# Kernel optimization log

Hardware: AMD Instinct MI355X
Metric: run time of the kernel (lower is better)

Reference implementation:

```python
import jax, jax.numpy as jnp
import numpy as np
from jax import lax

B, N, T, H = 128, 2, 256, 128  # batch, inc_nodes, seq_len, lstm hidden


def setup_inputs() -> dict:
    key = jax.random.key(0)
    ks = jax.random.split(key, 20)
    r = lambda i, shape, s: (jax.random.normal(ks[i], shape) * s).astype(jnp.float32)
    return {
        "x": r(0, (B, N, T), 1.0),
        "h0": r(1, (N, 4, B, H), 1.0),   # (node, layer*D+dir, B, H), torch.randn init states
        "c0": r(2, (N, 4, B, H), 1.0),
        "w_ih0": r(3, (N, 2, 4 * H, 1), 0.05),
        "w_hh0": r(4, (N, 2, 4 * H, H), 0.05),
        "b0": r(5, (N, 2, 4 * H), 0.05),
        "w_ih1": r(6, (N, 2, 4 * H, 2 * H), 0.05),
        "w_hh1": r(7, (N, 2, 4 * H, H), 0.05),
        "b1": r(8, (N, 2, 4 * H), 0.05),
        "w_fc0": r(9, (N * 2 * H, 256), 0.05), "b_fc0": r(10, (256,), 0.05),
        "ln0_a": r(11, (256,), 1.0), "ln0_b": r(12, (256,), 1.0),
        "w_fc1": r(13, (256, 256), 0.05), "b_fc1": r(14, (256,), 0.05),
        "ln1_a": r(15, (256,), 1.0), "ln1_b": r(16, (256,), 1.0),
        "w_fc2": r(17, (256, 64), 0.05), "b_fc2": r(18, (64,), 0.05),
    }


def _lstm_dir(xp, h0, c0, w_hh):
    # xp: [T, B, 4H] precomputed input projections + bias; returns [T, B, H]
    def step(hc, xt):
        h, c = hc
        g = xt + h @ w_hh.T
        i, f, gg, o = jnp.split(g, 4, axis=-1)  # torch gate order i,f,g,o
        c = jax.nn.sigmoid(f) * c + jax.nn.sigmoid(i) * jnp.tanh(gg)
        h = jax.nn.sigmoid(o) * jnp.tanh(c)
        return (h, c), h
    _, hs = lax.scan(step, (h0, c0), xp)
    return hs


def _bidir(x, h0, c0, w_ih, w_hh, b):
    # x: [B,T,Din]; h0,c0: [2,B,H]; w_ih: [2,4H,Din]; w_hh: [2,4H,H]; b: [2,4H]
    xp_f = jnp.moveaxis(x @ w_ih[0].T + b[0], 1, 0)            # [T,B,4H]
    hf = _lstm_dir(xp_f, h0[0], c0[0], w_hh[0])
    xp_b = jnp.moveaxis(x[:, ::-1] @ w_ih[1].T + b[1], 1, 0)
    hb = _lstm_dir(xp_b, h0[1], c0[1], w_hh[1])[::-1]
    return jnp.moveaxis(jnp.concatenate([hf, hb], axis=-1), 0, 1)  # [B,T,2H]


def _node(xn, h0n, c0n, wi0, wh0, bb0, wi1, wh1, bb1):
    # xn: [B,T,1]; h0n/c0n: [4,B,H] laid out (l0f, l0b, l1f, l1b)
    y = _bidir(xn, h0n[0:2], c0n[0:2], wi0, wh0, bb0)
    y = _bidir(y, h0n[2:4], c0n[2:4], wi1, wh1, bb1)
    return y[:, -1]  # last timestep, [B,2H]


def _layernorm(x, a, b, eps=1e-6):
    mu = jnp.mean(x, axis=-1, keepdims=True)
    std = jnp.std(x, axis=-1, keepdims=True, ddof=1) + eps  # torch.std is unbiased
    return (x - mu) / std * a + b


def reference(x, h0, c0, w_ih0, w_hh0, b0, w_ih1, w_hh1, b1,
              w_fc0, b_fc0, ln0_a, ln0_b, w_fc1, b_fc1, ln1_a, ln1_b, w_fc2, b_fc2):
    bsz = x.shape[0]
    xs = jnp.moveaxis(x, 1, 0)[..., None]  # [N,B,T,1]
    outs = jax.vmap(_node)(xs, h0, c0, w_ih0, w_hh0, b0, w_ih1, w_hh1, b1)  # [N,B,2H]
    t = jnp.moveaxis(outs, 0, 1).reshape(bsz, -1)  # hstack over nodes -> [B, N*2H]
    t = t @ w_fc0 + b_fc0
    t = jax.nn.relu(t + _layernorm(t, ln0_a, ln0_b))
    t = t @ w_fc1 + b_fc1
    t = jax.nn.relu(t + _layernorm(t, ln1_a, ln1_b))
    t = t @ w_fc2 + b_fc2
    return t.reshape(-1, 1, t.shape[-1])  # [B,1,out_dim]
```

## Files before the change

kernel.cpp:

```cpp
#include <hip/hip_runtime.h>
#include <hip/hip_fp16.h>

#define T_SEQ 256

typedef _Float16 half8 __attribute__((ext_vector_type(8)));
typedef float float4v __attribute__((ext_vector_type(4)));

__device__ __forceinline__ float fexp2(float x) { return __builtin_amdgcn_exp2f(x); }
__device__ __forceinline__ float frcp(float x) { return __builtin_amdgcn_rcpf(x); }
__device__ __forceinline__ float sigf(float x) { return frcp(1.f + fexp2(-1.4426950408889634f * x)); }
__device__ __forceinline__ float tanhf_(float x) { return 1.f - 2.f * frcp(1.f + fexp2(2.8853900817779268f * x)); }

__device__ __forceinline__ void relaxed_barrier() {
    __builtin_amdgcn_sched_barrier(0);
    asm volatile("s_waitcnt lgkmcnt(0)" ::: "memory");
    __builtin_amdgcn_s_barrier();
    asm volatile("" ::: "memory");
    __builtin_amdgcn_sched_barrier(0);
}

__global__ __launch_bounds__(512, 1) void lstm_l0(
    const float* __restrict__ x, const float* __restrict__ h0,
    const float* __restrict__ c0, const float* __restrict__ wih0,
    const float* __restrict__ whh0, const float* __restrict__ b0,
    _Float16* __restrict__ y0f) {
    const int wg = blockIdx.x;
    const int chain = wg >> 3, n = chain >> 1, d = chain & 1;
    const int bg = wg & 7, bbase = bg * 16;
    const int tid = threadIdx.x;
    const int wave = tid >> 6, lane = tid & 63, lrow = lane & 15, lgrp = lane >> 4;

    __shared__ __align__(16) float xsT[T_SEQ][16];
    __shared__ __align__(16) _Float16 hfrag[2][4][64][8];

    {
        int r = tid >> 5, ck = tid & 31;
        const float* xr = &x[((bbase + r) * 2 + n) * T_SEQ + ck * 8];
        float4v v0 = *(const float4v*)xr, v1 = *(const float4v*)(xr + 4);
#pragma unroll
        for (int i = 0; i < 4; ++i) { xsT[ck * 8 + i][r] = v0[i]; xsT[ck * 8 + 4 + i][r] = v1[i]; }
    }
    const int sidx = n * 4 + d;
    for (int idx = tid; idx < 256; idx += 512) {
        int kk = idx >> 6, l = idx & 63;
        int b = bbase + (l & 15), k0 = kk * 32 + (l >> 4) * 8;
        const float4v* s4 = (const float4v*)&h0[((size_t)(sidx * 128 + b)) * 128 + k0];
        float4v v0 = s4[0], v1 = s4[1];
        _Float16* dp = &hfrag[0][kk][l][0];
#pragma unroll
        for (int j = 0; j < 4; ++j) { dp[j] = (_Float16)v0[j]; dp[4 + j] = (_Float16)v1[j]; }
    }
    float wi[4], bi[4];
    half8 wf[4][4];
#pragma unroll
    for (int p = 0; p < 4; ++p) {
        int g = (wave + 8 * p) * 16 + lrow;
        wi[p] = wih0[chain * 512 + g];
        bi[p] = b0[chain * 512 + g];
        const float* sg = &whh0[(size_t)(chain * 512 + g) * 128];
#pragma unroll
        for (int kk = 0; kk < 4; ++kk) {
            const float4v* s4 = (const float4v*)&sg[kk * 32 + lgrp * 8];
            float4v v0 = s4[0], v1 = s4[1];
            half8 h;
#pragma unroll
            for (int j = 0; j < 4; ++j) { h[j] = (_Float16)v0[j]; h[4 + j] = (_Float16)v1[j]; }
            wf[p][kk] = h;
        }
    }
    const int hc = wave * 16 + lrow;
    float creg[4];
#pragma unroll
    for (int jj = 0; jj < 4; ++jj)
        creg[jj] = c0[((size_t)(sidx * 128 + bbase + 4 * lgrp + jj)) * 128 + hc];
    __syncthreads();

    const int kkst = d * 4 + (wave >> 1);
    const int lanehi = 16 * ((wave & 1) * 2 + (lrow >> 3));
    const int jst = lrow & 7;
    const int kkw = hc >> 5, lsub = (hc >> 3) & 3, jd = hc & 7;

    for (int t = 0; t < T_SEQ; ++t) {
        const int cur = t & 1, nxt = cur ^ 1;
        const int tx = d ? (T_SEQ - 1 - t) : t;
        half8 a[4];
#pragma unroll
        for (int kk = 0; kk < 4; ++kk) a[kk] = *(const half8*)&hfrag[cur][kk][lane][0];
        float4v xv = *(const float4v*)&xsT[tx][4 * lgrp];
        float4v acc[4];
#pragma unroll
        for (int p = 0; p < 4; ++p) {
#pragma unroll
            for (int jj = 0; jj < 4; ++jj) acc[p][jj] = fmaf(xv[jj], wi[p], bi[p]);
        }
#pragma unroll
        for (int kk = 0; kk < 4; ++kk)
#pragma unroll
            for (int p = 0; p < 4; ++p)
                acc[p] = __builtin_amdgcn_mfma_f32_16x16x32_f16(a[kk], wf[p][kk], acc[p], 0, 0, 0);

        _Float16* yb = &y0f[((((size_t)n * 256 + tx) * 8 + bg) * 8 + kkst) * 512 + (size_t)lanehi * 8 + jst];
#pragma unroll
        for (int jj = 0; jj < 4; ++jj) {
            float ig = sigf(acc[0][jj]), fg = sigf(acc[1][jj]);
            float gg = tanhf_(acc[2][jj]), og = sigf(acc[3][jj]);
            float c = fmaf(fg, creg[jj], ig * gg);
            creg[jj] = c;
            float ho = og * tanhf_(c);
            _Float16 hv = (_Float16)ho;
            hfrag[nxt][kkw][16 * lsub + 4 * lgrp + jj][jd] = hv;
            yb[(4 * lgrp + jj) * 8] = hv;
        }
        relaxed_barrier();
    }
}

__global__ __launch_bounds__(512, 1) void lstm_l1(
    const float* __restrict__ h0, const float* __restrict__ c0,
    const float* __restrict__ wih1, const float* __restrict__ whh1,
    const float* __restrict__ b1, const _Float16* __restrict__ y0f,
    float* __restrict__ lo) {
    const int wg = blockIdx.x;
    const int chain = wg >> 3, n = chain >> 1, d = chain & 1;
    const int bg = wg & 7, bbase = bg * 16;
    const int tid = threadIdx.x;
    const int wave = tid >> 6, lane = tid & 63, lrow = lane & 15, lgrp = lane >> 4;

    __shared__ __align__(16) _Float16 yfrag[2][8][64][8];
    __shared__ __align__(16) _Float16 hfrag[2][4][64][8];

    const int sidx = n * 4 + 2 + d;
    for (int idx = tid; idx < 256; idx += 512) {
        int kk = idx >> 6, l = idx & 63;
        int b = bbase + (l & 15), k0 = kk * 32 + (l >> 4) * 8;
        const float4v* s4 = (const float4v*)&h0[((size_t)(sidx * 128 + b)) * 128 + k0];
        float4v v0 = s4[0], v1 = s4[1];
        _Float16* dp = &hfrag[0][kk][l][0];
#pragma unroll
        for (int j = 0; j < 4; ++j) { dp[j] = (_Float16)v0[j]; dp[4 + j] = (_Float16)v1[j]; }
    }
    float bi[4];
    half8 wih[4][8];
    half8 wf[4][4];
#pragma unroll
    for (int p = 0; p < 4; ++p) {
        int g = (wave + 8 * p) * 16 + lrow;
        bi[p] = b1[chain * 512 + g];
        const float* sg = &wih1[(size_t)(chain * 512 + g) * 256];
#pragma unroll
        for (int kk = 0; kk < 8; ++kk) {
            const float4v* s4 = (const float4v*)&sg[kk * 32 + lgrp * 8];
            float4v v0 = s4[0], v1 = s4[1];
            half8 h;
#pragma unroll
            for (int j = 0; j < 4; ++j) { h[j] = (_Float16)v0[j]; h[4 + j] = (_Float16)v1[j]; }
            wih[p][kk] = h;
        }
        const float* sh = &whh1[(size_t)(chain * 512 + g) * 128];
#pragma unroll
        for (int kk = 0; kk < 4; ++kk) {
            const float4v* s4 = (const float4v*)&sh[kk * 32 + lgrp * 8];
            float4v v0 = s4[0], v1 = s4[1];
            half8 h;
#pragma unroll
            for (int j = 0; j < 4; ++j) { h[j] = (_Float16)v0[j]; h[4 + j] = (_Float16)v1[j]; }
            wf[p][kk] = h;
        }
    }
    const int hc = wave * 16 + lrow;
    float creg[4];
#pragma unroll
    for (int jj = 0; jj < 4; ++jj)
        creg[jj] = c0[((size_t)(sidx * 128 + bbase + 4 * lgrp + jj)) * 128 + hc];

    const int nsteps = d ? 1 : T_SEQ;
    const int t0 = d ? (T_SEQ - 1) : 0;
    {
        const half8* src = (const half8*)&y0f[(((size_t)n * 256 + t0) * 8 + bg) * 4096];
        ((half8*)&yfrag[0][0][0][0])[tid] = src[tid];
    }
    __syncthreads();

    const int kkw = hc >> 5, lsub = (hc >> 3) & 3, jd = hc & 7;

    for (int t = 0; t < nsteps; ++t) {
        const int cur = t & 1, nxt = cur ^ 1;
        const bool pf = (t + 1 < nsteps);
        half8 yreg;
        if (pf) {
            const half8* src = (const half8*)&y0f[(((size_t)n * 256 + (t + 1)) * 8 + bg) * 4096];
            yreg = src[tid];
        }
        float4v acc[4];
#pragma unroll
        for (int p = 0; p < 4; ++p) acc[p] = (float4v){bi[p], bi[p], bi[p], bi[p]};
        half8 fcur = *(const half8*)&yfrag[cur][0][lane][0];
#pragma unroll
        for (int kk = 0; kk < 12; ++kk) {
            half8 fnxt;
            if (kk < 7)       fnxt = *(const half8*)&yfrag[cur][kk + 1][lane][0];
            else if (kk < 11) fnxt = *(const half8*)&hfrag[cur][kk - 7][lane][0];
#pragma unroll
            for (int p = 0; p < 4; ++p) {
                half8 B = (kk < 8) ? wih[p][kk] : wf[p][kk - 8];
                acc[p] = __builtin_amdgcn_mfma_f32_16x16x32_f16(fcur, B, acc[p], 0, 0, 0);
            }
            if (kk < 11) fcur = fnxt;
        }
        float hout[4];
#pragma unroll
        for (int jj = 0; jj < 4; ++jj) {
            float ig = sigf(acc[0][jj]), fg = sigf(acc[1][jj]);
            float gg = tanhf_(acc[2][jj]), og = sigf(acc[3][jj]);
            float c = fmaf(fg, creg[jj], ig * gg);
            creg[jj] = c;
            hout[jj] = og * tanhf_(c);
        }
#pragma unroll
        for (int jj = 0; jj < 4; ++jj)
            hfrag[nxt][kkw][16 * lsub + 4 * lgrp + jj][jd] = (_Float16)hout[jj];
        if (pf) ((half8*)&yfrag[nxt][0][0][0])[tid] = yreg;
        if (t == nsteps - 1) {
#pragma unroll
            for (int jj = 0; jj < 4; ++jj)
                lo[(size_t)(bbase + 4 * lgrp + jj) * 512 + n * 256 + d * 128 + hc] = hout[jj];
        }
        relaxed_barrier();
    }
}

__global__ __launch_bounds__(256) void head_k(
    const float* __restrict__ lo,
    const float* __restrict__ w0, const float* __restrict__ bb0,
    const float* __restrict__ a0, const float* __restrict__ g0,
    const float* __restrict__ w1, const float* __restrict__ bb1,
    const float* __restrict__ a1, const float* __restrict__ g1,
    const float* __restrict__ w2, const float* __restrict__ bb2,
    float* __restrict__ out) {
    const int b = blockIdx.x, j = threadIdx.x;
    const int lane = j & 63, wid = j >> 6;
    __shared__ float row[512];
    __shared__ float buf[256];
    __shared__ float redA[4], redB[4];

    row[j] = lo[b * 512 + j];
    row[256 + j] = lo[b * 512 + 256 + j];
    __syncthreads();

    float s = bb0[j];
#pragma unroll 8
    for (int k = 0; k < 512; ++k) s = fmaf(row[k], w0[k * 256 + j], s);
    float v = s, v2 = s * s;
#pragma unroll
    for (int off = 32; off; off >>= 1) { v += __shfl_xor(v, off); v2 += __shfl_xor(v2, off); }
    if (lane == 0) { redA[wid] = v; redB[wid] = v2; }
    __syncthreads();
    float S = redA[0] + redA[1] + redA[2] + redA[3];
    float SS = redB[0] + redB[1] + redB[2] + redB[3];
    float mu = S * (1.f / 256.f);
    float var = (SS - S * mu) * (1.f / 255.f);
    float stdv = sqrtf(var) + 1e-6f;
    float t0 = fmaxf(s + (s - mu) / stdv * a0[j] + g0[j], 0.f);
    buf[j] = t0;
    __syncthreads();

    float s1 = bb1[j];
#pragma unroll 8
    for (int k = 0; k < 256; ++k) s1 = fmaf(buf[k], w1[k * 256 + j], s1);
    v = s1; v2 = s1 * s1;
#pragma unroll
    for (int off = 32; off; off >>= 1) { v += __shfl_xor(v, off); v2 += __shfl_xor(v2, off); }
    if (lane == 0) { redA[wid] = v; redB[wid] = v2; }
    __syncthreads();
    S = redA[0] + redA[1] + redA[2] + redA[3];
    SS = redB[0] + redB[1] + redB[2] + redB[3];
    mu = S * (1.f / 256.f);
    var = (SS - S * mu) * (1.f / 255.f);
    stdv = sqrtf(var) + 1e-6f;
    float t1 = fmaxf(s1 + (s1 - mu) / stdv * a1[j] + g1[j], 0.f);
    __syncthreads();
    buf[j] = t1;
    __syncthreads();

    if (j < 64) {
        float s2 = bb2[j];
#pragma unroll 8
        for (int k = 0; k < 256; ++k) s2 = fmaf(buf[k], w2[k * 64 + j], s2);
        out[b * 64 + j] = s2;
    }
}

extern "C" void kernel_launch(void* const* d_in, const int* in_sizes, int n_in,
                              void* d_out, int out_size, void* d_ws, size_t ws_size,
                              hipStream_t stream) {
    const float* x    = (const float*)d_in[0];
    const float* h0   = (const float*)d_in[1];
    const float* c0   = (const float*)d_in[2];
    const float* wih0 = (const float*)d_in[3];
    const float* whh0 = (const float*)d_in[4];
    const float* bb0  = (const float*)d_in[5];
    const float* wih1 = (const float*)d_in[6];
    const float* whh1 = (const float*)d_in[7];
    const float* bb1  = (const float*)d_in[8];
    const float* wfc0 = (const float*)d_in[9];
    const float* bfc0 = (const float*)d_in[10];
    const float* ln0a = (const float*)d_in[11];
    const float* ln0b = (const float*)d_in[12];
    const float* wfc1 = (const float*)d_in[13];
    const float* bfc1 = (const float*)d_in[14];
    const float* ln1a = (const float*)d_in[15];
    const float* ln1b = (const float*)d_in[16];
    const float* wfc2 = (const float*)d_in[17];
    const float* bfc2 = (const float*)d_in[18];

    char* ws = (char*)d_ws;
    _Float16* y0f = (_Float16*)ws;
    float*    lo  = (float*)(ws + (size_t)33554432);

    lstm_l0<<<dim3(32), dim3(512), 0, stream>>>(x, h0, c0, wih0, whh0, bb0, y0f);
    lstm_l1<<<dim3(32), dim3(512), 0, stream>>>(h0, c0, wih1, whh1, bb1, y0f, lo);
    head_k<<<dim3(128), dim3(256), 0, stream>>>(lo, wfc0, bfc0, ln0a, ln0b,
                                                wfc1, bfc1, ln1a, ln1b, wfc2, bfc2,
                                                (float*)d_out);
}
```

Before: 750.7 us.

## Store layer-0 outputs as whole LDS fragments and load layer-1 inputs via global_load_lds

```diff
diff --git a/kernel.cpp b/kernel.cpp
--- a/kernel.cpp
+++ b/kernel.cpp
@@ -11,9 +11,21 @@
 __device__ __forceinline__ float sigf(float x) { return frcp(1.f + fexp2(-1.4426950408889634f * x)); }
 __device__ __forceinline__ float tanhf_(float x) { return 1.f - 2.f * frcp(1.f + fexp2(2.8853900817779268f * x)); }
 
+__device__ __forceinline__ void gload_lds16(const void* g, void* l) {
+    __builtin_amdgcn_global_load_lds((const __attribute__((address_space(1))) void*)g,
+                                     (__attribute__((address_space(3))) void*)l, 16, 0, 0);
+}
+
 __device__ __forceinline__ void relaxed_barrier() {
     __builtin_amdgcn_sched_barrier(0);
     asm volatile("s_waitcnt lgkmcnt(0)" ::: "memory");
+    __builtin_amdgcn_s_barrier();
+    asm volatile("" ::: "memory");
+    __builtin_amdgcn_sched_barrier(0);
+}
+__device__ __forceinline__ void vm_barrier() {
+    __builtin_amdgcn_sched_barrier(0);
+    asm volatile("s_waitcnt vmcnt(0) lgkmcnt(0)" ::: "memory");
     __builtin_amdgcn_s_barrier();
     asm volatile("" ::: "memory");
     __builtin_amdgcn_sched_barrier(0);
@@ -75,9 +87,6 @@
         creg[jj] = c0[((size_t)(sidx * 128 + bbase + 4 * lgrp + jj)) * 128 + hc];
     __syncthreads();
 
-    const int kkst = d * 4 + (wave >> 1);
-    const int lanehi = 16 * ((wave & 1) * 2 + (lrow >> 3));
-    const int jst = lrow & 7;
     const int kkw = hc >> 5, lsub = (hc >> 3) & 3, jd = hc & 7;
 
     for (int t = 0; t < T_SEQ; ++t) {
@@ -86,6 +95,12 @@
         half8 a[4];
 #pragma unroll
         for (int kk = 0; kk < 4; ++kk) a[kk] = *(const half8*)&hfrag[cur][kk][lane][0];
+        if (t > 0 && tid < 256) {
+            const int txp = d ? (T_SEQ - t) : (t - 1);
+            half8 v = ((const half8*)&hfrag[cur][0][0][0])[tid];
+            half8* dst = (half8*)&y0f[((size_t)(n * 256 + txp) * 8 + bg) * 4096 + d * 2048];
+            dst[tid] = v;
+        }
         float4v xv = *(const float4v*)&xsT[tx][4 * lgrp];
         float4v acc[4];
 #pragma unroll
@@ -98,20 +113,21 @@
 #pragma unroll
             for (int p = 0; p < 4; ++p)
                 acc[p] = __builtin_amdgcn_mfma_f32_16x16x32_f16(a[kk], wf[p][kk], acc[p], 0, 0, 0);
-
-        _Float16* yb = &y0f[((((size_t)n * 256 + tx) * 8 + bg) * 8 + kkst) * 512 + (size_t)lanehi * 8 + jst];
 #pragma unroll
         for (int jj = 0; jj < 4; ++jj) {
             float ig = sigf(acc[0][jj]), fg = sigf(acc[1][jj]);
             float gg = tanhf_(acc[2][jj]), og = sigf(acc[3][jj]);
             float c = fmaf(fg, creg[jj], ig * gg);
             creg[jj] = c;
-            float ho = og * tanhf_(c);
-            _Float16 hv = (_Float16)ho;
-            hfrag[nxt][kkw][16 * lsub + 4 * lgrp + jj][jd] = hv;
-            yb[(4 * lgrp + jj) * 8] = hv;
+            hfrag[nxt][kkw][16 * lsub + 4 * lgrp + jj][jd] = (_Float16)(og * tanhf_(c));
         }
         relaxed_barrier();
+    }
+    if (tid < 256) {
+        const int txl = d ? 0 : (T_SEQ - 1);
+        half8 v = ((const half8*)&hfrag[0][0][0][0])[tid];
+        half8* dst = (half8*)&y0f[((size_t)(n * 256 + txl) * 8 + bg) * 4096 + d * 2048];
+        dst[tid] = v;
     }
 }
 
@@ -126,7 +142,7 @@
     const int tid = threadIdx.x;
     const int wave = tid >> 6, lane = tid & 63, lrow = lane & 15, lgrp = lane >> 4;
 
-    __shared__ __align__(16) _Float16 yfrag[2][8][64][8];
+    __shared__ __align__(16) _Float16 ybuf[2][4096];
     __shared__ __align__(16) _Float16 hfrag[2][4][64][8];
 
     const int sidx = n * 4 + 2 + d;
@@ -175,38 +191,36 @@
 
     const int nsteps = d ? 1 : T_SEQ;
     const int t0 = d ? (T_SEQ - 1) : 0;
-    {
-        const half8* src = (const half8*)&y0f[(((size_t)n * 256 + t0) * 8 + bg) * 4096];
-        ((half8*)&yfrag[0][0][0][0])[tid] = src[tid];
-    }
+    gload_lds16(&y0f[(((size_t)n * 256 + t0) * 8 + bg) * 4096 + (size_t)tid * 8],
+                &ybuf[0][wave * 512]);
+    asm volatile("s_waitcnt vmcnt(0)" ::: "memory");
     __syncthreads();
 
     const int kkw = hc >> 5, lsub = (hc >> 3) & 3, jd = hc & 7;
 
     for (int t = 0; t < nsteps; ++t) {
         const int cur = t & 1, nxt = cur ^ 1;
-        const bool pf = (t + 1 < nsteps);
-        half8 yreg;
-        if (pf) {
-            const half8* src = (const half8*)&y0f[(((size_t)n * 256 + (t + 1)) * 8 + bg) * 4096];
-            yreg = src[tid];
-        }
+        if (t + 1 < nsteps)
+            gload_lds16(&y0f[(((size_t)n * 256 + (t + 1)) * 8 + bg) * 4096 + (size_t)tid * 8],
+                        &ybuf[nxt][wave * 512]);
+        half8 ay[8], ah[4];
+#pragma unroll
+        for (int kk = 0; kk < 8; ++kk) ay[kk] = *(const half8*)&ybuf[cur][kk * 512 + lane * 8];
+#pragma unroll
+        for (int kk = 0; kk < 4; ++kk) ah[kk] = *(const half8*)&hfrag[cur][kk][lane][0];
         float4v acc[4];
 #pragma unroll
         for (int p = 0; p < 4; ++p) acc[p] = (float4v){bi[p], bi[p], bi[p], bi[p]};
-        half8 fcur = *(const half8*)&yfrag[cur][0][lane][0];
-#pragma unroll
-        for (int kk = 0; kk < 12; ++kk) {
-            half8 fnxt;
-            if (kk < 7)       fnxt = *(const half8*)&yfrag[cur][kk + 1][lane][0];
-            else if (kk < 11) fnxt = *(const half8*)&hfrag[cur][kk - 7][lane][0];
-#pragma unroll
-            for (int p = 0; p < 4; ++p) {
-                half8 B = (kk < 8) ? wih[p][kk] : wf[p][kk - 8];
-                acc[p] = __builtin_amdgcn_mfma_f32_16x16x32_f16(fcur, B, acc[p], 0, 0, 0);
-            }
-            if (kk < 11) fcur = fnxt;
-        }
+#pragma unroll
+        for (int kk = 0; kk < 8; ++kk)
+#pragma unroll
+            for (int p = 0; p < 4; ++p)
+                acc[p] = __builtin_amdgcn_mfma_f32_16x16x32_f16(ay[kk], wih[p][kk], acc[p], 0, 0, 0);
+#pragma unroll
+        for (int kk = 0; kk < 4; ++kk)
+#pragma unroll
+            for (int p = 0; p < 4; ++p)
+                acc[p] = __builtin_amdgcn_mfma_f32_16x16x32_f16(ah[kk], wf[p][kk], acc[p], 0, 0, 0);
         float hout[4];
 #pragma unroll
         for (int jj = 0; jj < 4; ++jj) {
@@ -219,13 +233,12 @@
 #pragma unroll
         for (int jj = 0; jj < 4; ++jj)
             hfrag[nxt][kkw][16 * lsub + 4 * lgrp + jj][jd] = (_Float16)hout[jj];
-        if (pf) ((half8*)&yfrag[nxt][0][0][0])[tid] = yreg;
         if (t == nsteps - 1) {
 #pragma unroll
             for (int jj = 0; jj < 4; ++jj)
                 lo[(size_t)(bbase + 4 * lgrp + jj) * 512 + n * 256 + d * 128 + hc] = hout[jj];
         }
-        relaxed_barrier();
+        vm_barrier();
     }
 }
 
```

Result: no change. 755.9 us (+0.7%).
